# Kernel tuning notes

Hardware: AMD Instinct MI355X
Metric: run time of the kernel (lower is better)

## Reference

```python
import jax, jax.numpy as jnp
import numpy as np

N, C, OUT, E, H = 4096, 256, 256, 131072, 8
DH = C // H
EPS = 1e-5


def layer_norm(h, g, b):
    mu = jnp.mean(h, axis=-1, keepdims=True)
    var = jnp.mean(jnp.square(h - mu), axis=-1, keepdims=True)
    return (h - mu) * jax.lax.rsqrt(var + EPS) * g + b


def setup_inputs() -> dict:
    key = jax.random.key(0)
    ks = jax.random.split(key, 12)
    s = 1.0 / np.sqrt(C)
    return {
        "x": jax.random.normal(ks[0], (N, C), jnp.float32),
        "edge_index": jax.random.randint(ks[1], (2, E), 0, N, jnp.int32),
        "edge_attr": jax.random.normal(ks[2], (E, C), jnp.float32),
        # nn.MultiheadAttention params
        "in_proj_w": jax.random.uniform(ks[3], (3 * C, C), jnp.float32, -s, s),
        "in_proj_b": jnp.zeros((3 * C,), jnp.float32),
        "attn_out_w": jax.random.uniform(ks[4], (C, C), jnp.float32, -s, s),
        "attn_out_b": jnp.zeros((C,), jnp.float32),
        # edge_mlp: Linear(3C -> OUT) + LayerNorm(OUT)
        "edge_w": jax.random.uniform(ks[5], (OUT, 3 * C), jnp.float32, -1 / np.sqrt(3 * C), 1 / np.sqrt(3 * C)),
        "edge_b": jax.random.uniform(ks[6], (OUT,), jnp.float32, -1 / np.sqrt(3 * C), 1 / np.sqrt(3 * C)),
        "ln1_g": jnp.ones((OUT,), jnp.float32),
        "ln1_b": jnp.zeros((OUT,), jnp.float32),
        # output_proj: Linear(C + OUT -> OUT)
        "out_w": jax.random.uniform(ks[7], (OUT, C + OUT), jnp.float32, -1 / np.sqrt(C + OUT), 1 / np.sqrt(C + OUT)),
        "out_b": jax.random.uniform(ks[8], (OUT,), jnp.float32, -1 / np.sqrt(C + OUT), 1 / np.sqrt(C + OUT)),
        "ln2_g": jnp.ones((OUT,), jnp.float32),
        "ln2_b": jnp.zeros((OUT,), jnp.float32),
    }


def reference(x, edge_index, edge_attr, in_proj_w, in_proj_b, attn_out_w, attn_out_b,
              edge_w, edge_b, ln1_g, ln1_b, out_w, out_b, ln2_g, ln2_b):
    num_nodes = x.shape[0]
    # --- dense self-attention over all nodes (seq len = N, batch 1) ---
    qkv = x @ in_proj_w.T + in_proj_b            # [N, 3C]
    q, k, v = jnp.split(qkv, 3, axis=-1)
    q = q.reshape(num_nodes, H, DH).transpose(1, 0, 2)  # [H, N, DH]
    k = k.reshape(num_nodes, H, DH).transpose(1, 0, 2)
    v = v.reshape(num_nodes, H, DH).transpose(1, 0, 2)
    scores = jnp.einsum("hqd,hkd->hqk", q, k) / np.sqrt(DH)
    attn = jax.nn.softmax(scores, axis=-1)       # dropout inactive at eval
    ctx = jnp.einsum("hqk,hkd->hqd", attn, v)    # [H, N, DH]
    ctx = ctx.transpose(1, 0, 2).reshape(num_nodes, C)
    x_attn = ctx @ attn_out_w.T + attn_out_b     # [N, C]
    # --- vectorized edge messages: gather -> MLP -> scatter-add ---
    row, col = edge_index[0], edge_index[1]
    msg_in = jnp.concatenate([x[row], x[col], edge_attr], axis=-1)  # [E, 3C]
    msg = jax.nn.relu(layer_norm(msg_in @ edge_w.T + edge_b, ln1_g, ln1_b))
    node_messages = jax.ops.segment_sum(msg, col, num_segments=num_nodes)  # [N, OUT]
    # --- combine, project, residual, norm ---
    combined = jnp.concatenate([x_attn, node_messages], axis=-1)
    out = combined @ out_w.T + out_b
    out = out + x                                # OUT == C so residual fires
    return layer_norm(out, ln2_g, ln2_b)
```

## Files before the change

### kernel.cpp

```cpp
#include <hip/hip_runtime.h>
#include <hip/hip_bf16.h>
#include <math.h>

typedef __bf16 bf16;
typedef __bf16 bf16x8 __attribute__((ext_vector_type(8)));
typedef __bf16 bf16x4 __attribute__((ext_vector_type(4)));
typedef float f32x4 __attribute__((ext_vector_type(4)));
typedef float f32x16 __attribute__((ext_vector_type(16)));

#define MFMA16(a, b, c) __builtin_amdgcn_mfma_f32_16x16x32_bf16((a), (b), (c), 0, 0, 0)
#define MFMA32(a, b, c) __builtin_amdgcn_mfma_f32_32x32x16_bf16((a), (b), (c), 0, 0, 0)

#define N_NODES 4096
#define C_DIM   256
#define E_EDGES 131072
#define APAD    280
#define TPAD    264

__device__ __forceinline__ float ldf(const void* p, int i, bool f32) {
    return f32 ? ((const float*)p)[i] : (float)((const bf16*)p)[i];
}

__device__ __forceinline__ bf16x8 ld8(const void* base, size_t off, bool f32) {
    if (f32) {
        const float* p = (const float*)base + off;
        float4 a = *(const float4*)p;
        float4 b = *(const float4*)(p + 4);
        bf16x8 r;
        r[0] = (bf16)a.x; r[1] = (bf16)a.y; r[2] = (bf16)a.z; r[3] = (bf16)a.w;
        r[4] = (bf16)b.x; r[5] = (bf16)b.y; r[6] = (bf16)b.z; r[7] = (bf16)b.w;
        return r;
    }
    return *(const bf16x8*)((const bf16*)base + off);
}

__device__ __forceinline__ unsigned cvtpk(float a, float b) {
    unsigned r;
    asm("v_cvt_pk_bf16_f32 %0, %1, %2" : "=v"(r) : "v"(a), "v"(b));
    return r;
}
__device__ __forceinline__ void pl32swap(unsigned &a, unsigned &b) {
    asm volatile("v_permlane32_swap_b32 %0, %1" : "+v"(a), "+v"(b));
}

union PW { unsigned u[4]; bf16x8 v; };

__global__ __launch_bounds__(64) void detect_dtype(const void* x, int* flag)
{
    const bf16* xb = (const bf16*)x;
    int tid = threadIdx.x;
    int bad = 0;
    for (int i = tid; i < 4096; i += 64) {
        float v = fabsf((float)xb[i]);
        if (!(v >= 1e-6f && v <= 100.0f)) bad++;
    }
#pragma unroll
    for (int m = 1; m < 64; m <<= 1) bad += __shfl_xor(bad, m);
    if (tid == 0) *flag = (bad > 400) ? 1 : 0;
}

__global__ __launch_bounds__(256) void convert_inputs(
    const void* s0, const void* s1, const void* s2, const void* s3, const void* s4,
    bf16* dst, const int* flag)
{
    int idx = blockIdx.x * 256 + threadIdx.x;
    const void* src; int local;
    if (idx < 1048576)      { src = s0; local = idx; }
    else if (idx < 1245184) { src = s1; local = idx - 1048576; }
    else if (idx < 1310720) { src = s2; local = idx - 1245184; }
    else if (idx < 1507328) { src = s3; local = idx - 1310720; }
    else                    { src = s4; local = idx - 1507328; }
    if (*flag) dst[idx] = (bf16)(((const float*)src)[local]);
    else ((unsigned short*)dst)[idx] = ((const unsigned short*)src)[local];
}

__global__ __launch_bounds__(256) void edge_hist(
    const int* __restrict__ ecol, int* __restrict__ counts)
{
    int e = blockIdx.x * 256 + threadIdx.x;
    atomicAdd(&counts[ecol[e]], 1);
}

__global__ __launch_bounds__(256) void edge_scan(
    const int* __restrict__ counts, int* __restrict__ offsets,
    int* __restrict__ cursor)
{
    __shared__ int part[256];
    __shared__ int pref[257];
    int t = threadIdx.x;
    int base = t * 16;
    int s = 0;
#pragma unroll
    for (int i = 0; i < 16; ++i) s += counts[base + i];
    part[t] = s;
    __syncthreads();
    if (t == 0) {
        int run = 0;
        for (int i = 0; i < 256; ++i) { pref[i] = run; run += part[i]; }
        pref[256] = run;
    }
    __syncthreads();
    int off = pref[t];
#pragma unroll
    for (int i = 0; i < 16; ++i) {
        offsets[base + i] = off;
        cursor[base + i]  = off;
        off += counts[base + i];
    }
    if (t == 255) offsets[4096] = off;
}

__global__ __launch_bounds__(256) void edge_scatter(
    const int* __restrict__ ecol, int* __restrict__ cursor,
    int* __restrict__ eid, int* __restrict__ epos)
{
    int e = blockIdx.x * 256 + threadIdx.x;
    int pos = atomicAdd(&cursor[ecol[e]], 1);
    eid[pos] = e;
    epos[e] = pos;
}

__global__ __launch_bounds__(256) void gemm_bt(
    const bf16* __restrict__ A, int lda,
    const bf16* __restrict__ W, int ldw,
    const void* __restrict__ bias,
    void* __restrict__ Cout, int ldc, int c_f32,
    const bf16* __restrict__ resid, int ldr,
    int K, const int* __restrict__ flag)
{
    const bool f32 = (*flag != 0);
    const int wave = threadIdx.x >> 6;
    const int lane = threadIdx.x & 63;
    const int quad = lane >> 4;
    const int l16  = lane & 15;
    const int m_base = blockIdx.x * 32;
    const int n_base = blockIdx.y * 256 + wave * 64;

    const bf16* a0p = A + (size_t)(m_base + l16) * lda + quad * 8;
    const bf16* a1p = a0p + (size_t)16 * lda;
    const bf16* wp  = W + (size_t)(n_base + l16) * ldw + quad * 8;

    f32x4 acc[2][4] = {};
    for (int k = 0; k < K; k += 32) {
        bf16x8 a0 = *(const bf16x8*)(a0p + k);
        bf16x8 a1 = *(const bf16x8*)(a1p + k);
#pragma unroll
        for (int nt = 0; nt < 4; ++nt) {
            bf16x8 b = *(const bf16x8*)(wp + (size_t)nt * 16 * ldw + k);
            acc[0][nt] = MFMA16(a0, b, acc[0][nt]);
            acc[1][nt] = MFMA16(a1, b, acc[1][nt]);
        }
    }
#pragma unroll
    for (int mt = 0; mt < 2; ++mt) {
#pragma unroll
        for (int nt = 0; nt < 4; ++nt) {
            int col = n_base + nt * 16 + l16;
            float bv = bias ? ldf(bias, col, f32) : 0.0f;
#pragma unroll
            for (int r = 0; r < 4; ++r) {
                int row = m_base + mt * 16 + quad * 4 + r;
                float v = acc[mt][nt][r] + bv;
                if (resid) v += (float)resid[(size_t)row * ldr + col];
                if (c_f32) ((float*)Cout)[(size_t)row * ldc + col] = v;
                else       ((bf16*)Cout)[(size_t)row * ldc + col] = (bf16)v;
            }
        }
    }
}

__global__ __launch_bounds__(256) void gemm_uv(
    const bf16* __restrict__ x, const bf16* __restrict__ ew,
    bf16* __restrict__ U, bf16* __restrict__ V)
{
    const int wave = threadIdx.x >> 6;
    const int lane = threadIdx.x & 63;
    const int quad = lane >> 4;
    const int l16  = lane & 15;
    const int m_base = blockIdx.x * 32;
    bf16* dst = blockIdx.y ? V : U;
    const bf16* W = ew + blockIdx.y * 256;

    const bf16* a0p = x + (size_t)(m_base + l16) * 256 + quad * 8;
    const bf16* a1p = a0p + (size_t)16 * 256;
    const bf16* wp  = W + (size_t)(wave * 64 + l16) * 768 + quad * 8;

    f32x4 acc[2][4] = {};
#pragma unroll
    for (int kk = 0; kk < 8; ++kk) {
        int k = kk * 32;
        bf16x8 a0 = *(const bf16x8*)(a0p + k);
        bf16x8 a1 = *(const bf16x8*)(a1p + k);
#pragma unroll
        for (int nt = 0; nt < 4; ++nt) {
            bf16x8 b = *(const bf16x8*)(wp + (size_t)nt * 16 * 768 + k);
            acc[0][nt] = MFMA16(a0, b, acc[0][nt]);
            acc[1][nt] = MFMA16(a1, b, acc[1][nt]);
        }
    }
#pragma unroll
    for (int mt = 0; mt < 2; ++mt)
#pragma unroll
        for (int nt = 0; nt < 4; ++nt) {
            int col = wave * 64 + nt * 16 + l16;
#pragma unroll
            for (int r = 0; r < 4; ++r) {
                int row = m_base + mt * 16 + quad * 4 + r;
                dst[(size_t)row * 256 + col] = (bf16)acc[mt][nt][r];
            }
        }
}

__global__ __launch_bounds__(256) void transpose_v(
    const bf16* __restrict__ qkv, bf16* __restrict__ vt)
{
    __shared__ bf16 t[32][65];
    const int n0 = blockIdx.x * 64;
    const int c0 = blockIdx.y * 32;
    const int tid = threadIdx.x;
    {
        int cl = tid & 31, nl = tid >> 5;
#pragma unroll
        for (int p = 0; p < 8; ++p) {
            int n = nl + p * 8;
            t[cl][n] = qkv[(size_t)(n0 + n) * 768 + 512 + c0 + cl];
        }
    }
    __syncthreads();
    {
        int nn = tid & 63, cc = tid >> 6;
#pragma unroll
        for (int p = 0; p < 8; ++p) {
            int c = cc + p * 4;
            vt[(size_t)(c0 + c) * 4096 + n0 + nn] = t[c][nn];
        }
    }
}

__global__ __launch_bounds__(256) void attn_kernel(
    const bf16* __restrict__ qkv,
    const bf16* __restrict__ vt,
    bf16* __restrict__ ctx)
{
    __shared__ float oL[4][32][33];
    __shared__ float mS[4][32];
    __shared__ float lS[4][32];
    const int tid  = threadIdx.x;
    const int wave = tid >> 6;
    const int lane = tid & 63;
    const int l32  = lane & 31;
    const int hl   = lane >> 5;
    const int h  = blockIdx.x >> 7;
    const int qt = blockIdx.x & 127;

    const float csc = 1.4426950408889634f * 0.17677669529663687f;

    const bf16* qrow = qkv + (size_t)(qt * 32 + l32) * 768 + h * 32 + hl * 8;
    bf16x8 qf1 = *(const bf16x8*)qrow;
    bf16x8 qf2 = *(const bf16x8*)(qrow + 16);

    const bf16* kbp = qkv + 256 + h * 32 + hl * 8;
    const bf16* vrp = vt + (size_t)(h * 32 + l32) * 4096 + hl * 8;

    float mrun = -INFINITY, msc = -INFINITY, lacc = 0.f;
    f32x16 oacc = {};
    const f32x16 z16 = {};

    const int kbeg = wave * 1024;
    for (int k0 = kbeg; k0 < kbeg + 1024; k0 += 32) {
        const bf16* kp = kbp + (size_t)(k0 + l32) * 768;
        bf16x8 kf1 = *(const bf16x8*)kp;
        bf16x8 kf2 = *(const bf16x8*)(kp + 16);
        bf16x8 vf1 = *(const bf16x8*)(vrp + k0);
        bf16x8 vf2 = *(const bf16x8*)(vrp + k0 + 16);

        f32x16 s = MFMA32(kf1, qf1, z16);
        s = MFMA32(kf2, qf2, s);

        float a0 = fmaxf(fmaxf(s[0], s[1]), fmaxf(s[2], s[3]));
        float a1 = fmaxf(fmaxf(s[4], s[5]), fmaxf(s[6], s[7]));
        float a2 = fmaxf(fmaxf(s[8], s[9]), fmaxf(s[10], s[11]));
        float a3 = fmaxf(fmaxf(s[12], s[13]), fmaxf(s[14], s[15]));
        float tm = fmaxf(fmaxf(a0, a1), fmaxf(a2, a3));
        tm = fmaxf(tm, __shfl_xor(tm, 32));

        if (__any(tm > mrun)) {
            float nm = fmaxf(mrun, tm);
            float nmsc = nm * csc;
            float al = exp2f(msc - nmsc);
            mrun = nm; msc = nmsc;
            lacc *= al;
#pragma unroll
            for (int i = 0; i < 16; ++i) oacc[i] *= al;
        }

        float p[16];
#pragma unroll
        for (int i = 0; i < 16; ++i) {
            p[i] = exp2f(__builtin_fmaf(s[i], csc, -msc));
            lacc += p[i];
        }

        unsigned w0 = cvtpk(p[0], p[1]),  w1 = cvtpk(p[2], p[3]);
        unsigned w2 = cvtpk(p[4], p[5]),  w3 = cvtpk(p[6], p[7]);
        unsigned w4 = cvtpk(p[8], p[9]),  w5 = cvtpk(p[10], p[11]);
        unsigned w6 = cvtpk(p[12], p[13]), w7 = cvtpk(p[14], p[15]);
        pl32swap(w0, w2); pl32swap(w1, w3);
        pl32swap(w4, w6); pl32swap(w5, w7);
        PW f1; f1.u[0] = w0; f1.u[1] = w1; f1.u[2] = w2; f1.u[3] = w3;
        PW f2; f2.u[0] = w4; f2.u[1] = w5; f2.u[2] = w6; f2.u[3] = w7;

        oacc = MFMA32(vf1, f1.v, oacc);
        oacc = MFMA32(vf2, f2.v, oacc);
    }

    lacc += __shfl_xor(lacc, 32);
    if (hl == 0) { mS[wave][l32] = mrun; lS[wave][l32] = lacc; }
#pragma unroll
    for (int i = 0; i < 16; ++i) {
        int d = (i & 3) + 8 * (i >> 2) + 4 * hl;
        oL[wave][l32][d] = oacc[i];
    }
    __syncthreads();
    {
        int q = tid >> 3, d0 = (tid & 7) * 4;
        float m0 = mS[0][q], m1 = mS[1][q], m2 = mS[2][q], m3 = mS[3][q];
        float ms = fmaxf(fmaxf(m0, m1), fmaxf(m2, m3));
        float f0 = exp2f((m0 - ms) * csc), f1 = exp2f((m1 - ms) * csc);
        float f2 = exp2f((m2 - ms) * csc), f3 = exp2f((m3 - ms) * csc);
        float ls = lS[0][q] * f0 + lS[1][q] * f1 + lS[2][q] * f2 + lS[3][q] * f3;
        float inv = 1.0f / ls;
        bf16x4 o4;
#pragma unroll
        for (int i = 0; i < 4; ++i) {
            int d = d0 + i;
            float v = (oL[0][q][d] * f0 + oL[1][q][d] * f1 +
                       oL[2][q][d] * f2 + oL[3][q][d] * f3) * inv;
            o4[i] = (bf16)v;
        }
        *(bf16x4*)(ctx + (size_t)(qt * 32 + q) * 256 + h * 32 + d0) = o4;
    }
}

__global__ __launch_bounds__(256, 4) void edge_gemm(
    const void* __restrict__ eattr,
    const bf16* __restrict__ ew,
    const void* __restrict__ eb,
    const int* __restrict__ epos,
    bf16* __restrict__ msgpre, const int* __restrict__ flag)
{
    __shared__ char smem[64 * APAD * 2];
    bf16* Asm = (bf16*)smem;
    float (*Trow)[TPAD] = (float(*)[TPAD])smem;

    const bool f32 = (*flag != 0);
    const int tid  = threadIdx.x;
    const int wave = tid >> 6;
    const int lane = tid & 63;
    const int quad = lane >> 4;
    const int l16  = lane & 15;
    const int e_base = blockIdx.x * 64;

    const bf16* wp = ew + (size_t)(wave * 64 + l16) * 768 + 512 + quad * 8;

    {
        int row   = tid >> 2;
        int cbase = (tid & 3) * 64;
        bf16* dst = Asm + row * APAD + cbase;
        if (!f32) {
            const bf16* src = (const bf16*)eattr + (size_t)(e_base + row) * 256 + cbase;
#pragma unroll
            for (int j = 0; j < 8; ++j)
                *(bf16x8*)(dst + j * 8) = *(const bf16x8*)(src + j * 8);
        } else {
            const float* src = (const float*)eattr + (size_t)(e_base + row) * 256 + cbase;
#pragma unroll
            for (int j = 0; j < 8; ++j) {
                float4 a = *(const float4*)(src + j * 8);
                float4 b = *(const float4*)(src + j * 8 + 4);
                bf16x8 r;
                r[0] = (bf16)a.x; r[1] = (bf16)a.y; r[2] = (bf16)a.z; r[3] = (bf16)a.w;
                r[4] = (bf16)b.x; r[5] = (bf16)b.y; r[6] = (bf16)b.z; r[7] = (bf16)b.w;
                *(bf16x8*)(dst + j * 8) = r;
            }
        }
    }
    __syncthreads();

    f32x4 acc[4][4] = {};
#pragma unroll
    for (int k0 = 0; k0 < 8; ++k0) {
        bf16x8 b[4];
#pragma unroll
        for (int nt = 0; nt < 4; ++nt)
            b[nt] = *(const bf16x8*)(wp + (size_t)nt * 16 * 768 + k0 * 32);
#pragma unroll
        for (int mt = 0; mt < 4; ++mt) {
            bf16x8 af = *(const bf16x8*)(Asm + (mt * 16 + l16) * APAD + k0 * 32 + quad * 8);
#pragma unroll
            for (int nt = 0; nt < 4; ++nt)
                acc[mt][nt] = MFMA16(af, b[nt], acc[mt][nt]);
        }
    }

    float ebv[4];
#pragma unroll
    for (int nt = 0; nt < 4; ++nt)
        ebv[nt] = ldf(eb, wave * 64 + nt * 16 + l16, f32);

    for (int p = 0; p < 2; ++p) {
        __syncthreads();
#pragma unroll
        for (int mtl = 0; mtl < 2; ++mtl) {
            int mt = p * 2 + mtl;
#pragma unroll
            for (int nt = 0; nt < 4; ++nt) {
                int c = wave * 64 + nt * 16 + l16;
                int cs = c ^ (((c >> 5) & 7) << 2);
#pragma unroll
                for (int r = 0; r < 4; ++r)
                    Trow[mtl * 16 + quad * 4 + r][cs] = acc[mt][nt][r] + ebv[nt];
            }
        }
        __syncthreads();
        {
            int row = tid >> 3;
            int seg = tid & 7;
            int ep = epos[e_base + p * 32 + row];
            const float* tr = Trow[row];
            const int t4 = (seg & 7) << 2;
            bf16* op = msgpre + (size_t)ep * 256 + seg * 32;
#pragma unroll
            for (int i = 0; i < 4; ++i) {
                float4 a = *(const float4*)(tr + ((seg * 32 + i * 8) ^ t4));
                float4 b = *(const float4*)(tr + ((seg * 32 + i * 8 + 4) ^ t4));
                bf16x8 o;
                o[0] = (bf16)a.x; o[1] = (bf16)a.y; o[2] = (bf16)a.z; o[3] = (bf16)a.w;
                o[4] = (bf16)b.x; o[5] = (bf16)b.y; o[6] = (bf16)b.z; o[7] = (bf16)b.w;
                *(bf16x8*)(op + i * 8) = o;
            }
        }
    }
}

__global__ __launch_bounds__(256) void node_ln(
    const bf16* __restrict__ msgpre,
    const int* __restrict__ offsets, const int* __restrict__ eid,
    const int* __restrict__ erow,
    const bf16* __restrict__ U, const bf16* __restrict__ V,
    const void* __restrict__ g1, const void* __restrict__ b1,
    bf16* __restrict__ combined, const int* __restrict__ flag)
{
    __shared__ float accL[4][256];
    const bool f32 = (*flag != 0);
    const int wave = threadIdx.x >> 6;
    const int lane = threadIdx.x & 63;
    const int node = blockIdx.x;
    const int start = offsets[node];
    const int cnt   = offsets[node + 1] - start;

    float glv[4], blv[4], vv[4];
#pragma unroll
    for (int i = 0; i < 4; ++i) {
        glv[i] = ldf(g1, lane * 4 + i, f32);
        blv[i] = ldf(b1, lane * 4 + i, f32);
    }
    {
        bf16x4 v4 = *(const bf16x4*)(V + (size_t)node * 256 + lane * 4);
#pragma unroll
        for (int i = 0; i < 4; ++i) vv[i] = (float)v4[i];
    }

    float nacc[4] = {0.f, 0.f, 0.f, 0.f};
    for (int i = wave; i < cnt; i += 4) {
        int pos = start + i;
        int er = erow[eid[pos]];
        bf16x4 t4 = *(const bf16x4*)(msgpre + (size_t)pos * 256 + lane * 4);
        bf16x4 u4 = *(const bf16x4*)(U + (size_t)er * 256 + lane * 4);
        float val[4];
        float s = 0.f, q = 0.f;
#pragma unroll
        for (int j = 0; j < 4; ++j) {
            val[j] = (float)t4[j] + (float)u4[j] + vv[j];
            s += val[j];
            q = __builtin_fmaf(val[j], val[j], q);
        }
#pragma unroll
        for (int msk = 1; msk < 64; msk <<= 1) {
            s += __shfl_xor(s, msk);
            q += __shfl_xor(q, msk);
        }
        float mean = s * (1.0f / 256.0f);
        float var  = q * (1.0f / 256.0f) - mean * mean;
        float rstd = rsqrtf(var + 1e-5f);
#pragma unroll
        for (int j = 0; j < 4; ++j)
            nacc[j] += fmaxf((val[j] - mean) * rstd * glv[j] + blv[j], 0.0f);
    }
#pragma unroll
    for (int j = 0; j < 4; ++j) accL[wave][lane * 4 + j] = nacc[j];
    __syncthreads();
    if (wave == 0) {
        bf16x4 o4;
#pragma unroll
        for (int j = 0; j < 4; ++j) {
            int c = lane * 4 + j;
            float s = (accL[0][c] + accL[1][c]) + (accL[2][c] + accL[3][c]);
            o4[j] = (bf16)s;
        }
        *(bf16x4*)(combined + (size_t)node * 512 + 256 + lane * 4) = o4;
    }
}

__global__ __launch_bounds__(256) void edge_node(
    const bf16* __restrict__ x,
    const int* __restrict__ erow,
    const void* __restrict__ eattr,
    const bf16* __restrict__ ew,
    const void* __restrict__ eb,
    const void* __restrict__ g1, const void* __restrict__ b1,
    const int* __restrict__ offsets, const int* __restrict__ eid,
    bf16* __restrict__ combined, const int* __restrict__ flag)
{
    __shared__ float part[32][4][2];
    const bool f32 = (*flag != 0);
    const int wave = threadIdx.x >> 6;
    const int lane = threadIdx.x & 63;
    const int quad = lane >> 4;
    const int l16  = lane & 15;
    const int n = blockIdx.x;
    const int start = offsets[n];
    const int cnt   = offsets[n + 1] - start;

    float gv[4], bv[4], ebv[4];
#pragma unroll
    for (int nt = 0; nt < 4; ++nt) {
        int col = wave * 64 + nt * 16 + l16;
        gv[nt]  = ldf(g1, col, f32);
        bv[nt]  = ldf(b1, col, f32);
        ebv[nt] = ldf(eb, col, f32);
    }
    const bf16* wp = ew + (size_t)(wave * 64 + l16) * 768 + quad * 8;
    const bf16* xn = x + (size_t)n * 256 + quad * 8;

    f32x4 acc1[4] = {};
#pragma unroll
    for (int kk = 0; kk < 8; ++kk) {
        bf16x8 a = *(const bf16x8*)(xn + kk * 32);
#pragma unroll
        for (int nt = 0; nt < 4; ++nt) {
            bf16x8 b = *(const bf16x8*)(wp + (size_t)nt * 16 * 768 + 256 + kk * 32);
            acc1[nt] = MFMA16(a, b, acc1[nt]);
        }
    }
    float nacc[4] = {0.f, 0.f, 0.f, 0.f};
    for (int c0 = 0; c0 < cnt; c0 += 32) {
        int i0 = c0 + l16;      i0 = (i0 < cnt) ? i0 : 0;
        int i1 = c0 + 16 + l16; i1 = (i1 < cnt) ? i1 : 0;
        int e0 = eid[start + i0];
        int e1 = eid[start + i1];
        const bf16* xr0 = x + (size_t)erow[e0] * 256 + quad * 8;
        const bf16* xr1 = x + (size_t)erow[e1] * 256 + quad * 8;
        f32x4 acc[2][4];
#pragma unroll
        for (int nt = 0; nt < 4; ++nt) { acc[0][nt] = acc1[nt]; acc[1][nt] = acc1[nt]; }
#pragma unroll
        for (int kk = 0; kk < 8; ++kk) {
            bf16x8 a0 = *(const bf16x8*)(xr0 + kk * 32);
            bf16x8 a1 = *(const bf16x8*)(xr1 + kk * 32);
#pragma unroll
            for (int nt = 0; nt < 4; ++nt) {
                bf16x8 b = *(const bf16x8*)(wp + (size_t)nt * 16 * 768 + kk * 32);
                acc[0][nt] = MFMA16(a0, b, acc[0][nt]);
                acc[1][nt] = MFMA16(a1, b, acc[1][nt]);
            }
        }
#pragma unroll
        for (int kk = 0; kk < 8; ++kk) {
            int koff = quad * 8 + kk * 32;
            bf16x8 a0 = ld8(eattr, (size_t)e0 * 256 + koff, f32);
            bf16x8 a1 = ld8(eattr, (size_t)e1 * 256 + koff, f32);
#pragma unroll
            for (int nt = 0; nt < 4; ++nt) {
                bf16x8 b = *(const bf16x8*)(wp + (size_t)nt * 16 * 768 + 512 + kk * 32);
                acc[0][nt] = MFMA16(a0, b, acc[0][nt]);
                acc[1][nt] = MFMA16(a1, b, acc[1][nt]);
            }
        }
#pragma unroll
        for (int mt = 0; mt < 2; ++mt)
#pragma unroll
            for (int nt = 0; nt < 4; ++nt)
#pragma unroll
                for (int r = 0; r < 4; ++r) acc[mt][nt][r] += ebv[nt];
        float ps[2][4], pq[2][4];
#pragma unroll
        for (int mt = 0; mt < 2; ++mt)
#pragma unroll
            for (int r = 0; r < 4; ++r) {
                float s = 0.f, q = 0.f;
#pragma unroll
                for (int nt = 0; nt < 4; ++nt) {
                    float v = acc[mt][nt][r];
                    s += v; q += v * v;
                }
                ps[mt][r] = s; pq[mt][r] = q;
            }
#pragma unroll
        for (int msk = 1; msk < 16; msk <<= 1)
#pragma unroll
            for (int mt = 0; mt < 2; ++mt)
#pragma unroll
                for (int r = 0; r < 4; ++r) {
                    ps[mt][r] += __shfl_xor(ps[mt][r], msk);
                    pq[mt][r] += __shfl_xor(pq[mt][r], msk);
                }
        if (l16 == 0) {
#pragma unroll
            for (int mt = 0; mt < 2; ++mt)
#pragma unroll
                for (int r = 0; r < 4; ++r) {
                    part[mt * 16 + quad * 4 + r][wave][0] = ps[mt][r];
                    part[mt * 16 + quad * 4 + r][wave][1] = pq[mt][r];
                }
        }
        __syncthreads();
#pragma unroll
        for (int mt = 0; mt < 2; ++mt)
#pragma unroll
            for (int r = 0; r < 4; ++r) {
                int row = mt * 16 + quad * 4 + r;
                float s = part[row][0][0] + part[row][1][0] + part[row][2][0] + part[row][3][0];
                float q = part[row][0][1] + part[row][1][1] + part[row][2][1] + part[row][3][1];
                float mean = s * (1.0f / 256.0f);
                float var  = q * (1.0f / 256.0f) - mean * mean;
                float rstd = rsqrtf(var + 1e-5f);
                if ((c0 + row) < cnt) {
#pragma unroll
                    for (int nt = 0; nt < 4; ++nt) {
                        float val = (acc[mt][nt][r] - mean) * rstd * gv[nt] + bv[nt];
                        nacc[nt] += fmaxf(val, 0.0f);
                    }
                }
            }
        __syncthreads();
    }
#pragma unroll
    for (int nt = 0; nt < 4; ++nt) {
        nacc[nt] += __shfl_xor(nacc[nt], 16);
        nacc[nt] += __shfl_xor(nacc[nt], 32);
    }
    if (quad == 0) {
#pragma unroll
        for (int nt = 0; nt < 4; ++nt)
            combined[(size_t)n * 512 + 256 + wave * 64 + nt * 16 + l16] = (bf16)nacc[nt];
    }
}

__global__ __launch_bounds__(256) void gemm_ln(
    const bf16* __restrict__ A,
    const bf16* __restrict__ W,
    const void* __restrict__ bias,
    const bf16* __restrict__ resid,
    const void* __restrict__ g, const void* __restrict__ bb,
    void* __restrict__ out, const int* __restrict__ flag)
{
    __shared__ float stats[16][4][2];
    const bool f32 = (*flag != 0);
    const int wave = threadIdx.x >> 6;
    const int lane = threadIdx.x & 63;
    const int quad = lane >> 4;
    const int l16  = lane & 15;
    const int m_base = blockIdx.x * 16;

    const bf16* ap = A + (size_t)(m_base + l16) * 512 + quad * 8;
    const bf16* wp = W + (size_t)(wave * 64 + l16) * 512 + quad * 8;

    f32x4 acc[4] = {};
#pragma unroll
    for (int kk = 0; kk < 16; ++kk) {
        int k = kk * 32;
        bf16x8 a = *(const bf16x8*)(ap + k);
#pragma unroll
        for (int nt = 0; nt < 4; ++nt) {
            bf16x8 b = *(const bf16x8*)(wp + (size_t)nt * 16 * 512 + k);
            acc[nt] = MFMA16(a, b, acc[nt]);
        }
    }
    float s[4] = {}, q[4] = {};
#pragma unroll
    for (int nt = 0; nt < 4; ++nt) {
        int col = wave * 64 + nt * 16 + l16;
        float bv = ldf(bias, col, f32);
#pragma unroll
        for (int r = 0; r < 4; ++r) {
            int row = m_base + quad * 4 + r;
            float v = acc[nt][r] + bv + (float)resid[(size_t)row * 256 + col];
            acc[nt][r] = v;
            s[r] += v;
            q[r] = __builtin_fmaf(v, v, q[r]);
        }
    }
#pragma unroll
    for (int msk = 1; msk < 16; msk <<= 1)
#pragma unroll
        for (int r = 0; r < 4; ++r) {
            s[r] += __shfl_xor(s[r], msk);
            q[r] += __shfl_xor(q[r], msk);
        }
    if (l16 == 0) {
#pragma unroll
        for (int r = 0; r < 4; ++r) {
            stats[quad * 4 + r][wave][0] = s[r];
            stats[quad * 4 + r][wave][1] = q[r];
        }
    }
    __syncthreads();
#pragma unroll
    for (int r = 0; r < 4; ++r) {
        int row16 = quad * 4 + r;
        float ss = (stats[row16][0][0] + stats[row16][1][0]) +
                   (stats[row16][2][0] + stats[row16][3][0]);
        float qq = (stats[row16][0][1] + stats[row16][1][1]) +
                   (stats[row16][2][1] + stats[row16][3][1]);
        float mean = ss * (1.0f / 256.0f);
        float var  = qq * (1.0f / 256.0f) - mean * mean;
        float rstd = rsqrtf(var + 1e-5f);
        int row = m_base + row16;
#pragma unroll
        for (int nt = 0; nt < 4; ++nt) {
            int col = wave * 64 + nt * 16 + l16;
            float o = (acc[nt][r] - mean) * rstd * ldf(g, col, f32) + ldf(bb, col, f32);
            if (f32) ((float*)out)[(size_t)row * 256 + col] = o;
            else     ((bf16*)out)[(size_t)row * 256 + col] = (bf16)o;
        }
    }
}

extern "C" void kernel_launch(void* const* d_in, const int* in_sizes, int n_in,
                              void* d_out, int out_size, void* d_ws, size_t ws_size,
                              hipStream_t stream)
{
    const void* x_raw  = d_in[0];
    const int*  eidx   = (const int*)d_in[1];
    const void* eattr  = d_in[2];
    const void* in_w   = d_in[3];
    const void* in_b   = d_in[4];
    const void* ao_w   = d_in[5];
    const void* ao_b   = d_in[6];
    const void* e_w    = d_in[7];
    const void* e_b    = d_in[8];
    const void* g1     = d_in[9];
    const void* b1     = d_in[10];
    const void* o_w    = d_in[11];
    const void* o_b    = d_in[12];
    const void* g2     = d_in[13];
    const void* b2     = d_in[14];

    char* ws = (char*)d_ws;
    bf16*  qkv      = (bf16*)(ws);
    bf16*  vt       = (bf16*)(ws + 6291456);
    bf16*  ctx      = (bf16*)(ws + 8388608);
    bf16*  combined = (bf16*)(ws + 10485760);
    int*   counts   = (int*)(ws + 14680064);
    int*   offsets  = (int*)(ws + 14696448);
    int*   cursor   = (int*)(ws + 14712848);
    int*   eid      = (int*)(ws + 14729232);
    int*   epos     = (int*)(ws + 15253520);
    bf16*  U        = (bf16*)(ws + 18874368);
    bf16*  V        = (bf16*)(ws + 20971520);
    bf16*  canon    = (bf16*)(ws + 23068672);
    int*   flag     = (int*)(ws + 26345472);
    bf16*  msgpre   = (bf16*)(ws + 26345728);

    const size_t WS_NEEDED = 93454592;

    bf16* x_bf   = canon;
    bf16* inw_bf = canon + 1048576;
    bf16* aow_bf = canon + 1245184;
    bf16* ew_bf  = canon + 1310720;
    bf16* ow_bf  = canon + 1507328;

    const int* erow = eidx;
    const int* ecol = eidx + E_EDGES;

    detect_dtype<<<dim3(1), 64, 0, stream>>>(x_raw, flag);
    convert_inputs<<<dim3(6400), 256, 0, stream>>>(x_raw, in_w, ao_w, e_w, o_w,
                                                   canon, flag);
    hipMemsetAsync(counts, 0, 16384, stream);
    edge_hist<<<dim3(E_EDGES / 256), 256, 0, stream>>>(ecol, counts);
    edge_scan<<<dim3(1), 256, 0, stream>>>(counts, offsets, cursor);
    edge_scatter<<<dim3(E_EDGES / 256), 256, 0, stream>>>(ecol, cursor, eid, epos);

    gemm_uv<<<dim3(128, 2), 256, 0, stream>>>(x_bf, ew_bf, U, V);

    gemm_bt<<<dim3(128, 3), 256, 0, stream>>>(x_bf, 256, inw_bf, 256, in_b,
                                              qkv, 768, 0, nullptr, 0, 256, flag);
    transpose_v<<<dim3(64, 8), 256, 0, stream>>>(qkv, vt);
    attn_kernel<<<dim3(1024), 256, 0, stream>>>(qkv, vt, ctx);
    gemm_bt<<<dim3(128, 1), 256, 0, stream>>>(ctx, 256, aow_bf, 256, ao_b,
                                              combined, 512, 0, nullptr, 0, 256, flag);
    if (ws_size >= WS_NEEDED) {
        edge_gemm<<<dim3(E_EDGES / 64), 256, 0, stream>>>(eattr, ew_bf, e_b,
                                                          epos, msgpre, flag);
        node_ln<<<dim3(N_NODES), 256, 0, stream>>>(msgpre, offsets, eid, erow,
                                                   U, V, g1, b1, combined, flag);
    } else {
        edge_node<<<dim3(N_NODES), 256, 0, stream>>>(x_bf, erow, eattr,
                                                     ew_bf, e_b, g1, b1,
                                                     offsets, eid, combined, flag);
    }
    gemm_ln<<<dim3(256), 256, 0, stream>>>(combined, ow_bf, o_b, x_bf,
                                           g2, b2, d_out, flag);
}
```

Measured before the change: 459.2 us.

## Make edge_gemm persistent over four tiles with register-prefetched edge_attr

Each edge_gemm block now handles four 64-edge tiles instead of one, so the grid shrinks fourfold. The next tile's edge_attr is loaded into registers while the current tile runs its MFMAs and scatter writes, then copied to LDS. The aim is to hide global load latency and spread the per-block setup cost (bias loads, launch) over more work. The cost is higher register pressure, now that the occupancy hint in launch_bounds is dropped, extra barriers per tile, and fewer blocks to balance across CUs.

```diff
diff --git a/kernel.cpp b/kernel.cpp
--- a/kernel.cpp
+++ b/kernel.cpp
@@ -16,6 +16,7 @@
 #define E_EDGES 131072
 #define APAD    280
 #define TPAD    264
+#define ETILES  4
 
 __device__ __forceinline__ float ldf(const void* p, int i, bool f32) {
     return f32 ? ((const float*)p)[i] : (float)((const bf16*)p)[i];
@@ -342,7 +343,7 @@
     }
 }
 
-__global__ __launch_bounds__(256, 4) void edge_gemm(
+__global__ __launch_bounds__(256) void edge_gemm(
     const void* __restrict__ eattr,
     const bf16* __restrict__ ew,
     const void* __restrict__ eb,
@@ -359,21 +360,29 @@
     const int lane = tid & 63;
     const int quad = lane >> 4;
     const int l16  = lane & 15;
-    const int e_base = blockIdx.x * 64;
+    const int srow  = tid >> 2;
+    const int cbase = (tid & 3) * 64;
 
     const bf16* wp = ew + (size_t)(wave * 64 + l16) * 768 + 512 + quad * 8;
 
+    float ebv[4];
+#pragma unroll
+    for (int nt = 0; nt < 4; ++nt)
+        ebv[nt] = ldf(eb, wave * 64 + nt * 16 + l16, f32);
+
+    const int tile0 = blockIdx.x * ETILES;
+
+    bf16x8 areg[8];
+
     {
-        int row   = tid >> 2;
-        int cbase = (tid & 3) * 64;
-        bf16* dst = Asm + row * APAD + cbase;
         if (!f32) {
-            const bf16* src = (const bf16*)eattr + (size_t)(e_base + row) * 256 + cbase;
-#pragma unroll
-            for (int j = 0; j < 8; ++j)
-                *(bf16x8*)(dst + j * 8) = *(const bf16x8*)(src + j * 8);
+            const bf16* src = (const bf16*)eattr +
+                (size_t)(tile0 * 64 + srow) * 256 + cbase;
+#pragma unroll
+            for (int j = 0; j < 8; ++j) areg[j] = *(const bf16x8*)(src + j * 8);
         } else {
-            const float* src = (const float*)eattr + (size_t)(e_base + row) * 256 + cbase;
+            const float* src = (const float*)eattr +
+                (size_t)(tile0 * 64 + srow) * 256 + cbase;
 #pragma unroll
             for (int j = 0; j < 8; ++j) {
                 float4 a = *(const float4*)(src + j * 8);
@@ -381,64 +390,95 @@
                 bf16x8 r;
                 r[0] = (bf16)a.x; r[1] = (bf16)a.y; r[2] = (bf16)a.z; r[3] = (bf16)a.w;
                 r[4] = (bf16)b.x; r[5] = (bf16)b.y; r[6] = (bf16)b.z; r[7] = (bf16)b.w;
-                *(bf16x8*)(dst + j * 8) = r;
-            }
-        }
+                areg[j] = r;
+            }
+        }
+        bf16* dst = Asm + srow * APAD + cbase;
+#pragma unroll
+        for (int j = 0; j < 8; ++j) *(bf16x8*)(dst + j * 8) = areg[j];
     }
     __syncthreads();
 
-    f32x4 acc[4][4] = {};
-#pragma unroll
-    for (int k0 = 0; k0 < 8; ++k0) {
-        bf16x8 b[4];
-#pragma unroll
-        for (int nt = 0; nt < 4; ++nt)
-            b[nt] = *(const bf16x8*)(wp + (size_t)nt * 16 * 768 + k0 * 32);
-#pragma unroll
-        for (int mt = 0; mt < 4; ++mt) {
-            bf16x8 af = *(const bf16x8*)(Asm + (mt * 16 + l16) * APAD + k0 * 32 + quad * 8);
+    for (int t = 0; t < ETILES; ++t) {
+        const int e_base = (tile0 + t) * 64;
+
+        if (t + 1 < ETILES) {
+            if (!f32) {
+                const bf16* src = (const bf16*)eattr +
+                    (size_t)((tile0 + t + 1) * 64 + srow) * 256 + cbase;
+#pragma unroll
+                for (int j = 0; j < 8; ++j) areg[j] = *(const bf16x8*)(src + j * 8);
+            } else {
+                const float* src = (const float*)eattr +
+                    (size_t)((tile0 + t + 1) * 64 + srow) * 256 + cbase;
+#pragma unroll
+                for (int j = 0; j < 8; ++j) {
+                    float4 a = *(const float4*)(src + j * 8);
+                    float4 b = *(const float4*)(src + j * 8 + 4);
+                    bf16x8 r;
+                    r[0] = (bf16)a.x; r[1] = (bf16)a.y; r[2] = (bf16)a.z; r[3] = (bf16)a.w;
+                    r[4] = (bf16)b.x; r[5] = (bf16)b.y; r[6] = (bf16)b.z; r[7] = (bf16)b.w;
+                    areg[j] = r;
+                }
+            }
+        }
+
+        f32x4 acc[4][4] = {};
+#pragma unroll
+        for (int k0 = 0; k0 < 8; ++k0) {
+            bf16x8 b[4];
 #pragma unroll
             for (int nt = 0; nt < 4; ++nt)
-                acc[mt][nt] = MFMA16(af, b[nt], acc[mt][nt]);
-        }
-    }
-
-    float ebv[4];
-#pragma unroll
-    for (int nt = 0; nt < 4; ++nt)
-        ebv[nt] = ldf(eb, wave * 64 + nt * 16 + l16, f32);
-
-    for (int p = 0; p < 2; ++p) {
-        __syncthreads();
-#pragma unroll
-        for (int mtl = 0; mtl < 2; ++mtl) {
-            int mt = p * 2 + mtl;
-#pragma unroll
-            for (int nt = 0; nt < 4; ++nt) {
-                int c = wave * 64 + nt * 16 + l16;
-                int cs = c ^ (((c >> 5) & 7) << 2);
-#pragma unroll
-                for (int r = 0; r < 4; ++r)
-                    Trow[mtl * 16 + quad * 4 + r][cs] = acc[mt][nt][r] + ebv[nt];
-            }
-        }
-        __syncthreads();
-        {
-            int row = tid >> 3;
-            int seg = tid & 7;
-            int ep = epos[e_base + p * 32 + row];
-            const float* tr = Trow[row];
-            const int t4 = (seg & 7) << 2;
-            bf16* op = msgpre + (size_t)ep * 256 + seg * 32;
-#pragma unroll
-            for (int i = 0; i < 4; ++i) {
-                float4 a = *(const float4*)(tr + ((seg * 32 + i * 8) ^ t4));
-                float4 b = *(const float4*)(tr + ((seg * 32 + i * 8 + 4) ^ t4));
-                bf16x8 o;
-                o[0] = (bf16)a.x; o[1] = (bf16)a.y; o[2] = (bf16)a.z; o[3] = (bf16)a.w;
-                o[4] = (bf16)b.x; o[5] = (bf16)b.y; o[6] = (bf16)b.z; o[7] = (bf16)b.w;
-                *(bf16x8*)(op + i * 8) = o;
-            }
+                b[nt] = *(const bf16x8*)(wp + (size_t)nt * 16 * 768 + k0 * 32);
+#pragma unroll
+            for (int mt = 0; mt < 4; ++mt) {
+                bf16x8 af = *(const bf16x8*)(Asm + (mt * 16 + l16) * APAD + k0 * 32 + quad * 8);
+#pragma unroll
+                for (int nt = 0; nt < 4; ++nt)
+                    acc[mt][nt] = MFMA16(af, b[nt], acc[mt][nt]);
+            }
+        }
+
+        for (int p = 0; p < 2; ++p) {
+            __syncthreads();
+#pragma unroll
+            for (int mtl = 0; mtl < 2; ++mtl) {
+                int mt = p * 2 + mtl;
+#pragma unroll
+                for (int nt = 0; nt < 4; ++nt) {
+                    int c = wave * 64 + nt * 16 + l16;
+                    int cs = c ^ (((c >> 5) & 7) << 2);
+#pragma unroll
+                    for (int r = 0; r < 4; ++r)
+                        Trow[mtl * 16 + quad * 4 + r][cs] = acc[mt][nt][r] + ebv[nt];
+                }
+            }
+            __syncthreads();
+            {
+                int row = tid >> 3;
+                int seg = tid & 7;
+                int ep = epos[e_base + p * 32 + row];
+                const float* tr = Trow[row];
+                const int t4 = (seg & 7) << 2;
+                bf16* op = msgpre + (size_t)ep * 256 + seg * 32;
+#pragma unroll
+                for (int i = 0; i < 4; ++i) {
+                    float4 a = *(const float4*)(tr + ((seg * 32 + i * 8) ^ t4));
+                    float4 b = *(const float4*)(tr + ((seg * 32 + i * 8 + 4) ^ t4));
+                    bf16x8 o;
+                    o[0] = (bf16)a.x; o[1] = (bf16)a.y; o[2] = (bf16)a.z; o[3] = (bf16)a.w;
+                    o[4] = (bf16)b.x; o[5] = (bf16)b.y; o[6] = (bf16)b.z; o[7] = (bf16)b.w;
+                    *(bf16x8*)(op + i * 8) = o;
+                }
+            }
+        }
+
+        if (t + 1 < ETILES) {
+            __syncthreads();
+            bf16* dst = Asm + srow * APAD + cbase;
+#pragma unroll
+            for (int j = 0; j < 8; ++j) *(bf16x8*)(dst + j * 8) = areg[j];
+            __syncthreads();
         }
     }
 }
@@ -801,8 +841,8 @@
     gemm_bt<<<dim3(128, 1), 256, 0, stream>>>(ctx, 256, aow_bf, 256, ao_b,
                                               combined, 512, 0, nullptr, 0, 256, flag);
     if (ws_size >= WS_NEEDED) {
-        edge_gemm<<<dim3(E_EDGES / 64), 256, 0, stream>>>(eattr, ew_bf, e_b,
-                                                          epos, msgpre, flag);
+        edge_gemm<<<dim3(E_EDGES / 64 / ETILES), 256, 0, stream>>>(eattr, ew_bf, e_b,
+                                                                   epos, msgpre, flag);
         node_ln<<<dim3(N_NODES), 256, 0, stream>>>(msgpre, offsets, eid, erow,
                                                    U, V, g1, b1, combined, flag);
     } else {
```

New measurement: 467.9 us. About the same (+1.9%).
